# Performance work log

Measured on AMD Instinct MI355X. Metric: run time of the kernel, lower is better.

## Reference

```python
import jax, jax.numpy as jnp
import numpy as np

EPS = 1e-6


def _safe_norm(x, axis, keepdims=True):
    # sqrt with zero-safe gradient (double-where trick)
    sq = (x * x).sum(axis=axis, keepdims=keepdims)
    safe = jnp.where(sq > 0, sq, 1.0)
    return jnp.where(sq > 0, jnp.sqrt(safe), 0.0)


def _complex_coord_norm(lig, pro, lig_mask, pro_mask, set_weights):
    # 'length' norm over the joint complex: scale each set so the mean vector
    # length over all real (lig + pro) nodes is ~1, with a learnable per-set weight.
    lig_len = _safe_norm(lig, axis=-1, keepdims=False) * lig_mask   # [B,S,Nl]
    pro_len = _safe_norm(pro, axis=-1, keepdims=False) * pro_mask   # [B,S,Np]
    total_len = lig_len.sum(-1) + pro_len.sum(-1)                   # [B,S]
    n_atoms = lig_mask.sum(-1) + pro_mask.sum(-1)                   # [B,S]
    mean_len = (total_len / n_atoms)[..., None, None]               # [B,S,1,1]
    w = set_weights[None, :, None, None]
    lig = lig * w / (mean_len + EPS) * lig_mask[..., None]
    pro = pro * w / (mean_len + EPS) * pro_mask[..., None]
    return lig, pro


def setup_inputs() -> dict:
    key = jax.random.key(0)
    ks = jax.random.split(key, 8)
    B, S, P, Nl, Np = 8, 64, 64, 128, 256
    scale = 1.0 / np.sqrt(S)
    return {
        "lig_coord_sets": jax.random.normal(ks[0], (B, S, Nl, 3), jnp.float32),
        "messages": jax.random.normal(ks[1], (B, Nl, Nl + Np, P), jnp.float32),
        "adj_matrix": jax.random.randint(ks[2], (B, Nl, Nl + Np), 0, 2, jnp.int32),
        "lig_node_mask": jnp.ones((B, S, Nl), jnp.float32),
        "pro_coord_sets": jax.random.normal(ks[3], (B, S, Np, 3), jnp.float32),
        "pro_node_mask": jnp.ones((B, S, Np), jnp.float32),
        "lig_proj_w": jax.random.normal(ks[4], (P, S), jnp.float32) * scale,
        "pro_proj_w": jax.random.normal(ks[5], (P, S), jnp.float32) * scale,
        "attn_proj_w": jax.random.normal(ks[6], (S, P), jnp.float32) * scale,
        "set_weights": jnp.ones((S,), jnp.float32),
    }


def reference(lig_coord_sets, messages, adj_matrix, lig_node_mask,
              pro_coord_sets, pro_node_mask,
              lig_proj_w, pro_proj_w, attn_proj_w, set_weights):
    B, S, Nl, _ = lig_coord_sets.shape
    lig, pro = _complex_coord_norm(lig_coord_sets, pro_coord_sets,
                                   lig_node_mask, pro_node_mask, set_weights)
    # Linear over the sets dim: [B,S,N,3] -> [B,3,N,P]
    lig_p = jnp.einsum('bsnc,ps->bcnp', lig, lig_proj_w)
    pro_p = jnp.einsum('bsnc,ps->bcnp', pro, pro_proj_w)
    proj = jnp.concatenate([lig_p, pro_p], axis=2)        # [B,3,N,P]
    # pairwise vector diffs, ligand queries only (matches post-hoc slice in torch)
    vec = proj[:, :, :Nl, None, :] - proj[:, :, None, :, :]   # [B,3,Nl,N,P]
    lengths = _safe_norm(vec, axis=1)                          # [B,1,Nl,N,P]
    norm_dists = vec / (lengths + EPS)
    attn_mask = jnp.where(adj_matrix > 0, 0.0, -jnp.inf)       # [B,Nl,N]
    attn = jax.nn.softmax(messages + attn_mask[..., None], axis=2)  # [B,Nl,N,P]
    upd = jnp.einsum('bcinp,binp->bcip', norm_dists, attn)     # [B,3,Nl,P]
    weights = jnp.sqrt((attn * attn).sum(axis=2))              # [B,Nl,P]
    upd = upd * weights[:, None]
    # attn_proj (P -> S) + transpose(1,-1): [B,3,Nl,P] -> [B,S,Nl,3]
    return jnp.einsum('bcip,sp->bsic', upd, attn_proj_w)
```

## Files before the change

kernel.cpp:

```cpp
#include <hip/hip_runtime.h>
#include <hip/hip_bf16.h>
#include <math.h>

#define B   8
#define S   64
#define NL  128
#define NPRO 256
#define NN  384
#define P   64
#define NGRP 8
#define EPSF 1e-6f

__global__ __launch_bounds__(64) void meanlen_kernel(
    const float* __restrict__ lig, const float* __restrict__ ligmask,
    const float* __restrict__ pro, const float* __restrict__ promask,
    float* __restrict__ meanlen)
{
    int blk = blockIdx.x;
    int t = threadIdx.x;
    float suml = 0.f, cnt = 0.f;

    const float* lbase = lig + (size_t)blk * NL * 3;
    const float* lm    = ligmask + (size_t)blk * NL;
    for (int n = t; n < NL; n += 64) {
        float x = lbase[n*3+0], y = lbase[n*3+1], z = lbase[n*3+2];
        float mk = lm[n];
        suml += sqrtf(x*x + y*y + z*z) * mk;
        cnt  += mk;
    }
    const float* pbase = pro + (size_t)blk * NPRO * 3;
    const float* pm    = promask + (size_t)blk * NPRO;
    for (int n = t; n < NPRO; n += 64) {
        float x = pbase[n*3+0], y = pbase[n*3+1], z = pbase[n*3+2];
        float mk = pm[n];
        suml += sqrtf(x*x + y*y + z*z) * mk;
        cnt  += mk;
    }
    for (int off = 32; off > 0; off >>= 1) {
        suml += __shfl_down(suml, off);
        cnt  += __shfl_down(cnt,  off);
    }
    if (t == 0) meanlen[blk] = suml / cnt;
}

__global__ __launch_bounds__(64) void proj_kernel(
    const float* __restrict__ lig, const float* __restrict__ pro,
    const float* __restrict__ ligmask, const float* __restrict__ promask,
    const float* __restrict__ ligw, const float* __restrict__ prow,
    const float* __restrict__ sw, const float* __restrict__ meanlen,
    float* __restrict__ projx, float* __restrict__ projy, float* __restrict__ projz)
{
    int blk = blockIdx.x;
    int b = blk / (NN / NGRP);
    int g = blk - b * (NN / NGRP);
    int nbase = g * NGRP;
    int t = threadIdx.x;
    bool isl = (nbase < NL);

    __shared__ float wl[64][65];
    const float* w = isl ? ligw : prow;
    for (int row = 0; row < 64; ++row) wl[row][t] = w[row * 64 + t];

    __shared__ float cs[NGRP][3][64];
    {
        int s = t;
        float gfac = sw[s] / (meanlen[b * S + s] + EPSF);
        for (int nn = 0; nn < NGRP; ++nn) {
            int n = nbase + nn;
            float mk, X, Y, Z;
            if (isl) {
                size_t base = ((size_t)b * S + s) * NL + n;
                mk = ligmask[base];
                X = lig[base*3+0]; Y = lig[base*3+1]; Z = lig[base*3+2];
            } else {
                size_t base = ((size_t)b * S + s) * NPRO + (n - NL);
                mk = promask[base];
                X = pro[base*3+0]; Y = pro[base*3+1]; Z = pro[base*3+2];
            }
            float gg = gfac * mk;
            cs[nn][0][s] = X * gg;
            cs[nn][1][s] = Y * gg;
            cs[nn][2][s] = Z * gg;
        }
    }
    __syncthreads();

    for (int nn = 0; nn < NGRP; ++nn) {
        float a0 = 0.f, a1 = 0.f, a2 = 0.f;
        #pragma unroll 8
        for (int s = 0; s < 64; ++s) {
            float wv = wl[t][s];
            a0 += cs[nn][0][s] * wv;
            a1 += cs[nn][1][s] * wv;
            a2 += cs[nn][2][s] * wv;
        }
        size_t base = ((size_t)b * NN + nbase + nn) * P;
        projx[base + t] = a0;
        projy[base + t] = a1;
        projz[base + t] = a2;
    }
}

#define PROC(C) { \
    float d0 = xix.C - xx.C, d1 = xiy.C - yy.C, d2 = xiz.C - zz.C; \
    float sq = fmaf(d0, d0, fmaf(d1, d1, d2 * d2)); \
    float inv; asm("v_rsq_f32 %0, %1" : "=v"(inv) : "v"(sq)); \
    inv = sq > 0.f ? inv : 0.f; \
    float xe = fmaf(mm.C, 1.44269504f, am); \
    float e; asm("v_exp_f32 %0, %1" : "=v"(e) : "v"(xe)); \
    S1.C += e; S2.C = fmaf(e, e, S2.C); \
    float ei = e * inv; \
    A0.C = fmaf(ei, d0, A0.C); \
    A1.C = fmaf(ei, d1, A1.C); \
    A2.C = fmaf(ei, d2, A2.C); }

#define RED(V) { V.x += __shfl_xor(V.x, off); V.y += __shfl_xor(V.y, off); \
                 V.z += __shfl_xor(V.z, off); V.w += __shfl_xor(V.w, off); }

__global__ __launch_bounds__(512) void attn_kernel(
    const float* __restrict__ messages,
    const int*   __restrict__ adj,
    const float* __restrict__ projx,
    const float* __restrict__ projy,
    const float* __restrict__ projz,
    const float* __restrict__ attn_w,
    float* __restrict__ out)
{
    int blk = blockIdx.x;
    int b = blk >> 7;
    int i = blk & (NL - 1);
    int t = threadIdx.x;
    int lane = t & 63;
    int wave = t >> 6;
    int pg = lane & 15;
    int wsl = lane >> 4;
    int slice = wave * 4 + wsl;

    __shared__ float amask[NN];
    __shared__ float ls1[8][64], ls2[8][64];
    __shared__ float la0[8][64], la1[8][64], la2[8][64];
    __shared__ float upd[3][64];

    const int* adj_base = adj + (size_t)blk * NN;
    for (int n = t; n < NN; n += 512)
        amask[n] = adj_base[n] > 0 ? 0.f : -INFINITY;

    const float4* m4  = (const float4*)messages + (size_t)blk * NN * 16;
    const float4* px4 = (const float4*)projx + (size_t)b * NN * 16;
    const float4* py4 = (const float4*)projy + (size_t)b * NN * 16;
    const float4* pz4 = (const float4*)projz + (size_t)b * NN * 16;

    float4 xix = px4[(size_t)i * 16 + pg];
    float4 xiy = py4[(size_t)i * 16 + pg];
    float4 xiz = pz4[(size_t)i * 16 + pg];

    __syncthreads();

    float4 S1 = {0,0,0,0}, S2 = {0,0,0,0};
    float4 A0 = {0,0,0,0}, A1 = {0,0,0,0}, A2 = {0,0,0,0};

    int nb = slice * 12;
    size_t idx0 = (size_t)nb * 16 + pg;
    float4 mc = m4[idx0], xc = px4[idx0], yc = py4[idx0], zc = pz4[idx0];

    #pragma unroll
    for (int k = 0; k < 12; ++k) {
        int n = nb + k;
        float4 mm = mc, xx = xc, yy = yc, zz = zc;
        if (k < 11) {
            size_t idx = (size_t)(n + 1) * 16 + pg;
            mc = m4[idx]; xc = px4[idx]; yc = py4[idx]; zc = pz4[idx];
        }
        float am = amask[n];
        PROC(x) PROC(y) PROC(z) PROC(w)
    }

    #pragma unroll
    for (int off = 16; off <= 32; off <<= 1) {
        RED(S1) RED(S2) RED(A0) RED(A1) RED(A2)
    }

    if (wsl == 0) {
        int pbase = pg * 4;
        ls1[wave][pbase+0] = S1.x; ls1[wave][pbase+1] = S1.y; ls1[wave][pbase+2] = S1.z; ls1[wave][pbase+3] = S1.w;
        ls2[wave][pbase+0] = S2.x; ls2[wave][pbase+1] = S2.y; ls2[wave][pbase+2] = S2.z; ls2[wave][pbase+3] = S2.w;
        la0[wave][pbase+0] = A0.x; la0[wave][pbase+1] = A0.y; la0[wave][pbase+2] = A0.z; la0[wave][pbase+3] = A0.w;
        la1[wave][pbase+0] = A1.x; la1[wave][pbase+1] = A1.y; la1[wave][pbase+2] = A1.z; la1[wave][pbase+3] = A1.w;
        la2[wave][pbase+0] = A2.x; la2[wave][pbase+1] = A2.y; la2[wave][pbase+2] = A2.z; la2[wave][pbase+3] = A2.w;
    }
    __syncthreads();

    if (t < 64) {
        float s1 = 0.f, s2 = 0.f, a0 = 0.f, a1 = 0.f, a2 = 0.f;
        #pragma unroll
        for (int w = 0; w < 8; ++w) {
            s1 += ls1[w][t]; s2 += ls2[w][t];
            a0 += la0[w][t]; a1 += la1[w][t]; a2 += la2[w][t];
        }
        float wgt = sqrtf(s2) / (s1 * s1);
        upd[0][t] = a0 * wgt;
        upd[1][t] = a1 * wgt;
        upd[2][t] = a2 * wgt;
    }
    __syncthreads();

    if (t < 192) {
        int s = t & 63, c = t >> 6;
        const float4* aw4 = (const float4*)attn_w + (size_t)s * 16;
        float o = 0.f;
        #pragma unroll
        for (int q = 0; q < 16; ++q) {
            float4 w4 = aw4[q];
            o = fmaf(upd[c][q*4+0], w4.x, o);
            o = fmaf(upd[c][q*4+1], w4.y, o);
            o = fmaf(upd[c][q*4+2], w4.z, o);
            o = fmaf(upd[c][q*4+3], w4.w, o);
        }
        out[(((size_t)b * S + s) * NL + i) * 3 + c] = o;
    }
}

extern "C" void kernel_launch(void* const* d_in, const int* in_sizes, int n_in,
                              void* d_out, int out_size, void* d_ws, size_t ws_size,
                              hipStream_t stream)
{
    const float* lig      = (const float*)d_in[0];
    const float* messages = (const float*)d_in[1];
    const int*   adj      = (const int*)  d_in[2];
    const float* ligmask  = (const float*)d_in[3];
    const float* pro      = (const float*)d_in[4];
    const float* promask  = (const float*)d_in[5];
    const float* ligw     = (const float*)d_in[6];
    const float* prow     = (const float*)d_in[7];
    const float* attnw    = (const float*)d_in[8];
    const float* sw       = (const float*)d_in[9];
    float* out = (float*)d_out;

    const size_t plane = (size_t)B * NN * P;
    float* meanlen = (float*)d_ws;
    float* projx   = (float*)((char*)d_ws + 2048);
    float* projy   = projx + plane;
    float* projz   = projy + plane;

    meanlen_kernel<<<B * S, 64, 0, stream>>>(lig, ligmask, pro, promask, meanlen);
    proj_kernel<<<B * (NN / NGRP), 64, 0, stream>>>(lig, pro, ligmask, promask,
                                                    ligw, prow, sw, meanlen,
                                                    projx, projy, projz);
    attn_kernel<<<B * NL, 512, 0, stream>>>(messages, adj, projx, projy, projz,
                                            attnw, out);
}
```

Baseline: 53.80 us.

## Process two query rows per attention block to reuse projected neighbor loads

The attention kernel now handles two ligand query rows per block, sharing the loads of projected neighbor coordinates between them and halving the grid. Prefetching is deepened to two iterations, and the zero-length guard is replaced by clamping rsq with fminf. This reduces redundant L2 reads of the proj planes and per-block overhead, at the cost of doubled accumulator registers and possibly lower occupancy.

```diff
diff --git a/kernel.cpp b/kernel.cpp
--- a/kernel.cpp
+++ b/kernel.cpp
@@ -101,18 +101,25 @@
     }
 }
 
-#define PROC(C) { \
-    float d0 = xix.C - xx.C, d1 = xiy.C - yy.C, d2 = xiz.C - zz.C; \
+#define PROC2(C) { \
+    float d0 = xi0x.C - xx.C, d1 = xi0y.C - yy.C, d2 = xi0z.C - zz.C; \
     float sq = fmaf(d0, d0, fmaf(d1, d1, d2 * d2)); \
     float inv; asm("v_rsq_f32 %0, %1" : "=v"(inv) : "v"(sq)); \
-    inv = sq > 0.f ? inv : 0.f; \
-    float xe = fmaf(mm.C, 1.44269504f, am); \
+    inv = fminf(inv, 1e30f); \
+    float xe = fmaf(mm0.C, 1.44269504f, am0); \
     float e; asm("v_exp_f32 %0, %1" : "=v"(e) : "v"(xe)); \
-    S1.C += e; S2.C = fmaf(e, e, S2.C); \
+    S1a.C += e; S2a.C = fmaf(e, e, S2a.C); \
     float ei = e * inv; \
-    A0.C = fmaf(ei, d0, A0.C); \
-    A1.C = fmaf(ei, d1, A1.C); \
-    A2.C = fmaf(ei, d2, A2.C); }
+    A0a.C = fmaf(ei, d0, A0a.C); A1a.C = fmaf(ei, d1, A1a.C); A2a.C = fmaf(ei, d2, A2a.C); \
+    d0 = xi1x.C - xx.C; d1 = xi1y.C - yy.C; d2 = xi1z.C - zz.C; \
+    sq = fmaf(d0, d0, fmaf(d1, d1, d2 * d2)); \
+    asm("v_rsq_f32 %0, %1" : "=v"(inv) : "v"(sq)); \
+    inv = fminf(inv, 1e30f); \
+    xe = fmaf(mm1.C, 1.44269504f, am1); \
+    asm("v_exp_f32 %0, %1" : "=v"(e) : "v"(xe)); \
+    S1b.C += e; S2b.C = fmaf(e, e, S2b.C); \
+    ei = e * inv; \
+    A0b.C = fmaf(ei, d0, A0b.C); A1b.C = fmaf(ei, d1, A1b.C); A2b.C = fmaf(ei, d2, A2b.C); }
 
 #define RED(V) { V.x += __shfl_xor(V.x, off); V.y += __shfl_xor(V.y, off); \
                  V.z += __shfl_xor(V.z, off); V.w += __shfl_xor(V.w, off); }
@@ -127,8 +134,10 @@
     float* __restrict__ out)
 {
     int blk = blockIdx.x;
-    int b = blk >> 7;
-    int i = blk & (NL - 1);
+    int b = blk >> 6;
+    int ip = blk & 63;
+    int i0 = ip * 2;
+    int i1 = i0 + 1;
     int t = threadIdx.x;
     int lane = t & 63;
     int wave = t >> 6;
@@ -136,85 +145,104 @@
     int wsl = lane >> 4;
     int slice = wave * 4 + wsl;
 
-    __shared__ float amask[NN];
-    __shared__ float ls1[8][64], ls2[8][64];
-    __shared__ float la0[8][64], la1[8][64], la2[8][64];
-    __shared__ float upd[3][64];
-
-    const int* adj_base = adj + (size_t)blk * NN;
-    for (int n = t; n < NN; n += 512)
-        amask[n] = adj_base[n] > 0 ? 0.f : -INFINITY;
-
-    const float4* m4  = (const float4*)messages + (size_t)blk * NN * 16;
+    __shared__ float amask[2][NN];
+    __shared__ __align__(16) float red[2][5][8][64];
+    __shared__ float upd[2][3][64];
+
+    const int* adj0 = adj + ((size_t)b * NL + i0) * NN;
+    const int* adj1 = adj + ((size_t)b * NL + i1) * NN;
+    for (int n = t; n < NN; n += 512) {
+        amask[0][n] = adj0[n] > 0 ? 0.f : -INFINITY;
+        amask[1][n] = adj1[n] > 0 ? 0.f : -INFINITY;
+    }
+
+    const float4* m04 = (const float4*)messages + ((size_t)b * NL + i0) * NN * 16;
+    const float4* m14 = (const float4*)messages + ((size_t)b * NL + i1) * NN * 16;
     const float4* px4 = (const float4*)projx + (size_t)b * NN * 16;
     const float4* py4 = (const float4*)projy + (size_t)b * NN * 16;
     const float4* pz4 = (const float4*)projz + (size_t)b * NN * 16;
 
-    float4 xix = px4[(size_t)i * 16 + pg];
-    float4 xiy = py4[(size_t)i * 16 + pg];
-    float4 xiz = pz4[(size_t)i * 16 + pg];
-
-    __syncthreads();
-
-    float4 S1 = {0,0,0,0}, S2 = {0,0,0,0};
-    float4 A0 = {0,0,0,0}, A1 = {0,0,0,0}, A2 = {0,0,0,0};
+    float4 xi0x = px4[(size_t)i0 * 16 + pg];
+    float4 xi0y = py4[(size_t)i0 * 16 + pg];
+    float4 xi0z = pz4[(size_t)i0 * 16 + pg];
+    float4 xi1x = px4[(size_t)i1 * 16 + pg];
+    float4 xi1y = py4[(size_t)i1 * 16 + pg];
+    float4 xi1z = pz4[(size_t)i1 * 16 + pg];
+
+    __syncthreads();
+
+    float4 S1a = {0,0,0,0}, S2a = {0,0,0,0}, A0a = {0,0,0,0}, A1a = {0,0,0,0}, A2a = {0,0,0,0};
+    float4 S1b = {0,0,0,0}, S2b = {0,0,0,0}, A0b = {0,0,0,0}, A1b = {0,0,0,0}, A2b = {0,0,0,0};
 
     int nb = slice * 12;
-    size_t idx0 = (size_t)nb * 16 + pg;
-    float4 mc = m4[idx0], xc = px4[idx0], yc = py4[idx0], zc = pz4[idx0];
+    size_t base = (size_t)nb * 16 + pg;
+
+    float4 bm0[2], bm1[2], bx[2], by[2], bz[2];
+    bm0[0] = m04[base];      bm1[0] = m14[base];
+    bx[0]  = px4[base];      by[0]  = py4[base];      bz[0] = pz4[base];
+    bm0[1] = m04[base + 16]; bm1[1] = m14[base + 16];
+    bx[1]  = px4[base + 16]; by[1]  = py4[base + 16]; bz[1] = pz4[base + 16];
 
     #pragma unroll
     for (int k = 0; k < 12; ++k) {
+        float4 mm0 = bm0[k & 1], mm1 = bm1[k & 1];
+        float4 xx = bx[k & 1], yy = by[k & 1], zz = bz[k & 1];
+        if (k < 10) {
+            size_t idx = base + (size_t)(k + 2) * 16;
+            bm0[k & 1] = m04[idx]; bm1[k & 1] = m14[idx];
+            bx[k & 1]  = px4[idx]; by[k & 1]  = py4[idx]; bz[k & 1] = pz4[idx];
+        }
         int n = nb + k;
-        float4 mm = mc, xx = xc, yy = yc, zz = zc;
-        if (k < 11) {
-            size_t idx = (size_t)(n + 1) * 16 + pg;
-            mc = m4[idx]; xc = px4[idx]; yc = py4[idx]; zc = pz4[idx];
-        }
-        float am = amask[n];
-        PROC(x) PROC(y) PROC(z) PROC(w)
+        float am0 = amask[0][n], am1 = amask[1][n];
+        PROC2(x) PROC2(y) PROC2(z) PROC2(w)
     }
 
     #pragma unroll
     for (int off = 16; off <= 32; off <<= 1) {
-        RED(S1) RED(S2) RED(A0) RED(A1) RED(A2)
+        RED(S1a) RED(S2a) RED(A0a) RED(A1a) RED(A2a)
+        RED(S1b) RED(S2b) RED(A0b) RED(A1b) RED(A2b)
     }
 
     if (wsl == 0) {
-        int pbase = pg * 4;
-        ls1[wave][pbase+0] = S1.x; ls1[wave][pbase+1] = S1.y; ls1[wave][pbase+2] = S1.z; ls1[wave][pbase+3] = S1.w;
-        ls2[wave][pbase+0] = S2.x; ls2[wave][pbase+1] = S2.y; ls2[wave][pbase+2] = S2.z; ls2[wave][pbase+3] = S2.w;
-        la0[wave][pbase+0] = A0.x; la0[wave][pbase+1] = A0.y; la0[wave][pbase+2] = A0.z; la0[wave][pbase+3] = A0.w;
-        la1[wave][pbase+0] = A1.x; la1[wave][pbase+1] = A1.y; la1[wave][pbase+2] = A1.z; la1[wave][pbase+3] = A1.w;
-        la2[wave][pbase+0] = A2.x; la2[wave][pbase+1] = A2.y; la2[wave][pbase+2] = A2.z; la2[wave][pbase+3] = A2.w;
-    }
-    __syncthreads();
-
-    if (t < 64) {
+        int pb = pg * 4;
+        *(float4*)&red[0][0][wave][pb] = S1a; *(float4*)&red[0][1][wave][pb] = S2a;
+        *(float4*)&red[0][2][wave][pb] = A0a; *(float4*)&red[0][3][wave][pb] = A1a;
+        *(float4*)&red[0][4][wave][pb] = A2a;
+        *(float4*)&red[1][0][wave][pb] = S1b; *(float4*)&red[1][1][wave][pb] = S2b;
+        *(float4*)&red[1][2][wave][pb] = A0b; *(float4*)&red[1][3][wave][pb] = A1b;
+        *(float4*)&red[1][4][wave][pb] = A2b;
+    }
+    __syncthreads();
+
+    if (t < 128) {
+        int il = t >> 6, p = t & 63;
         float s1 = 0.f, s2 = 0.f, a0 = 0.f, a1 = 0.f, a2 = 0.f;
         #pragma unroll
         for (int w = 0; w < 8; ++w) {
-            s1 += ls1[w][t]; s2 += ls2[w][t];
-            a0 += la0[w][t]; a1 += la1[w][t]; a2 += la2[w][t];
+            s1 += red[il][0][w][p]; s2 += red[il][1][w][p];
+            a0 += red[il][2][w][p]; a1 += red[il][3][w][p]; a2 += red[il][4][w][p];
         }
         float wgt = sqrtf(s2) / (s1 * s1);
-        upd[0][t] = a0 * wgt;
-        upd[1][t] = a1 * wgt;
-        upd[2][t] = a2 * wgt;
-    }
-    __syncthreads();
-
-    if (t < 192) {
-        int s = t & 63, c = t >> 6;
+        upd[il][0][p] = a0 * wgt;
+        upd[il][1][p] = a1 * wgt;
+        upd[il][2][p] = a2 * wgt;
+    }
+    __syncthreads();
+
+    if (t < 384) {
+        int il = t >= 192;
+        int r = t - il * 192;
+        int s = r & 63, c = r >> 6;
+        int i = i0 + il;
         const float4* aw4 = (const float4*)attn_w + (size_t)s * 16;
         float o = 0.f;
         #pragma unroll
         for (int q = 0; q < 16; ++q) {
             float4 w4 = aw4[q];
-            o = fmaf(upd[c][q*4+0], w4.x, o);
-            o = fmaf(upd[c][q*4+1], w4.y, o);
-            o = fmaf(upd[c][q*4+2], w4.z, o);
-            o = fmaf(upd[c][q*4+3], w4.w, o);
+            o = fmaf(upd[il][c][q*4+0], w4.x, o);
+            o = fmaf(upd[il][c][q*4+1], w4.y, o);
+            o = fmaf(upd[il][c][q*4+2], w4.z, o);
+            o = fmaf(upd[il][c][q*4+3], w4.w, o);
         }
         out[(((size_t)b * S + s) * NL + i) * 3 + c] = o;
     }
@@ -246,6 +274,6 @@
     proj_kernel<<<B * (NN / NGRP), 64, 0, stream>>>(lig, pro, ligmask, promask,
                                                     ligw, prow, sw, meanlen,
                                                     projx, projy, projz);
-    attn_kernel<<<B * NL, 512, 0, stream>>>(messages, adj, projx, projy, projz,
-                                            attnw, out);
-}
+    attn_kernel<<<B * NL / 2, 512, 0, stream>>>(messages, adj, projx, projy, projz,
+                                                attnw, out);
+}
```

New measurement: 52.88 us. Within noise of the previous version (-1.7%).

## Stream messages through double-buffered LDS tiles via global_load_lds in attn kernel

Applied to the files above, without the earlier changes.

The attention kernel now uses 256 threads per block and streams the messages tensor in 32-node tiles into double-buffered shared memory with direct global-to-LDS loads, prefetching the next tile while the current one is processed. Each 16-thread group handles two nodes per tile, and the cross-wave reduction buffers are packed into one float4-written array. The zero-length guard becomes a clamp of the rsq result. The intent is to hide latency on the dominant messages read. It adds a block-wide barrier per tile and halves the threads per block.

```diff
diff --git a/kernel.cpp b/kernel.cpp
--- a/kernel.cpp
+++ b/kernel.cpp
@@ -101,23 +101,24 @@
     }
 }
 
-#define PROC(C) { \
+#define NTILE 32
+#define TILES (NN / NTILE)
+
+#define PROC(mm, am, xx, yy, zz, C) { \
     float d0 = xix.C - xx.C, d1 = xiy.C - yy.C, d2 = xiz.C - zz.C; \
     float sq = fmaf(d0, d0, fmaf(d1, d1, d2 * d2)); \
     float inv; asm("v_rsq_f32 %0, %1" : "=v"(inv) : "v"(sq)); \
-    inv = sq > 0.f ? inv : 0.f; \
+    inv = fminf(inv, 1e30f); \
     float xe = fmaf(mm.C, 1.44269504f, am); \
     float e; asm("v_exp_f32 %0, %1" : "=v"(e) : "v"(xe)); \
     S1.C += e; S2.C = fmaf(e, e, S2.C); \
     float ei = e * inv; \
-    A0.C = fmaf(ei, d0, A0.C); \
-    A1.C = fmaf(ei, d1, A1.C); \
-    A2.C = fmaf(ei, d2, A2.C); }
+    A0.C = fmaf(ei, d0, A0.C); A1.C = fmaf(ei, d1, A1.C); A2.C = fmaf(ei, d2, A2.C); }
 
 #define RED(V) { V.x += __shfl_xor(V.x, off); V.y += __shfl_xor(V.y, off); \
                  V.z += __shfl_xor(V.z, off); V.w += __shfl_xor(V.w, off); }
 
-__global__ __launch_bounds__(512) void attn_kernel(
+__global__ __launch_bounds__(256) void attn_kernel(
     const float* __restrict__ messages,
     const int*   __restrict__ adj,
     const float* __restrict__ projx,
@@ -132,20 +133,20 @@
     int t = threadIdx.x;
     int lane = t & 63;
     int wave = t >> 6;
-    int pg = lane & 15;
+    int pg  = t & 15;
+    int sub = t >> 4;
     int wsl = lane >> 4;
-    int slice = wave * 4 + wsl;
 
     __shared__ float amask[NN];
-    __shared__ float ls1[8][64], ls2[8][64];
-    __shared__ float la0[8][64], la1[8][64], la2[8][64];
+    __shared__ __align__(16) float msgT[2][NTILE * P];
+    __shared__ __align__(16) float red[4][5][64];
     __shared__ float upd[3][64];
 
-    const int* adj_base = adj + (size_t)blk * NN;
-    for (int n = t; n < NN; n += 512)
-        amask[n] = adj_base[n] > 0 ? 0.f : -INFINITY;
-
-    const float4* m4  = (const float4*)messages + (size_t)blk * NN * 16;
+    const int* adjb = adj + (size_t)blk * NN;
+    for (int n = t; n < NN; n += 256)
+        amask[n] = adjb[n] > 0 ? 0.f : -INFINITY;
+
+    const float* msgb = messages + (size_t)blk * NN * P;
     const float4* px4 = (const float4*)projx + (size_t)b * NN * 16;
     const float4* py4 = (const float4*)projy + (size_t)b * NN * 16;
     const float4* pz4 = (const float4*)projz + (size_t)b * NN * 16;
@@ -154,25 +155,43 @@
     float4 xiy = py4[(size_t)i * 16 + pg];
     float4 xiz = pz4[(size_t)i * 16 + pg];
 
+    #define STAGE(buf, tile) { \
+        const char* gs = (const char*)(msgb + (size_t)(tile) * (NTILE * P)); \
+        char* ls = (char*)&msgT[buf][0] + wave * 2048; \
+        unsigned lo = wave * 2048 + lane * 16; \
+        __builtin_amdgcn_global_load_lds((const unsigned int*)(gs + lo), \
+                                         (unsigned int*)ls, 16, 0, 0); \
+        __builtin_amdgcn_global_load_lds((const unsigned int*)(gs + lo + 1024), \
+                                         (unsigned int*)(ls + 1024), 16, 0, 0); \
+    }
+
+    STAGE(0, 0)
     __syncthreads();
 
     float4 S1 = {0,0,0,0}, S2 = {0,0,0,0};
     float4 A0 = {0,0,0,0}, A1 = {0,0,0,0}, A2 = {0,0,0,0};
 
-    int nb = slice * 12;
-    size_t idx0 = (size_t)nb * 16 + pg;
-    float4 mc = m4[idx0], xc = px4[idx0], yc = py4[idx0], zc = pz4[idx0];
-
+    int cur = 0;
     #pragma unroll
-    for (int k = 0; k < 12; ++k) {
-        int n = nb + k;
-        float4 mm = mc, xx = xc, yy = yc, zz = zc;
-        if (k < 11) {
-            size_t idx = (size_t)(n + 1) * 16 + pg;
-            mc = m4[idx]; xc = px4[idx]; yc = py4[idx]; zc = pz4[idx];
-        }
-        float am = amask[n];
-        PROC(x) PROC(y) PROC(z) PROC(w)
+    for (int tile = 0; tile < TILES; ++tile) {
+        if (tile < TILES - 1) STAGE(cur ^ 1, tile + 1)
+
+        int n0 = tile * NTILE + sub * 2;
+        float4 mA = *(const float4*)&msgT[cur][(sub * 2    ) * P + pg * 4];
+        float4 mB = *(const float4*)&msgT[cur][(sub * 2 + 1) * P + pg * 4];
+        float amA = amask[n0], amB = amask[n0 + 1];
+
+        size_t gA = (size_t)n0 * 16 + pg;
+        float4 xA = px4[gA],      yA = py4[gA],      zA = pz4[gA];
+        float4 xB = px4[gA + 16], yB = py4[gA + 16], zB = pz4[gA + 16];
+
+        PROC(mA, amA, xA, yA, zA, x) PROC(mA, amA, xA, yA, zA, y)
+        PROC(mA, amA, xA, yA, zA, z) PROC(mA, amA, xA, yA, zA, w)
+        PROC(mB, amB, xB, yB, zB, x) PROC(mB, amB, xB, yB, zB, y)
+        PROC(mB, amB, xB, yB, zB, z) PROC(mB, amB, xB, yB, zB, w)
+
+        __syncthreads();
+        cur ^= 1;
     }
 
     #pragma unroll
@@ -181,21 +200,19 @@
     }
 
     if (wsl == 0) {
-        int pbase = pg * 4;
-        ls1[wave][pbase+0] = S1.x; ls1[wave][pbase+1] = S1.y; ls1[wave][pbase+2] = S1.z; ls1[wave][pbase+3] = S1.w;
-        ls2[wave][pbase+0] = S2.x; ls2[wave][pbase+1] = S2.y; ls2[wave][pbase+2] = S2.z; ls2[wave][pbase+3] = S2.w;
-        la0[wave][pbase+0] = A0.x; la0[wave][pbase+1] = A0.y; la0[wave][pbase+2] = A0.z; la0[wave][pbase+3] = A0.w;
-        la1[wave][pbase+0] = A1.x; la1[wave][pbase+1] = A1.y; la1[wave][pbase+2] = A1.z; la1[wave][pbase+3] = A1.w;
-        la2[wave][pbase+0] = A2.x; la2[wave][pbase+1] = A2.y; la2[wave][pbase+2] = A2.z; la2[wave][pbase+3] = A2.w;
+        int pb = pg * 4;
+        *(float4*)&red[wave][0][pb] = S1; *(float4*)&red[wave][1][pb] = S2;
+        *(float4*)&red[wave][2][pb] = A0; *(float4*)&red[wave][3][pb] = A1;
+        *(float4*)&red[wave][4][pb] = A2;
     }
     __syncthreads();
 
     if (t < 64) {
         float s1 = 0.f, s2 = 0.f, a0 = 0.f, a1 = 0.f, a2 = 0.f;
         #pragma unroll
-        for (int w = 0; w < 8; ++w) {
-            s1 += ls1[w][t]; s2 += ls2[w][t];
-            a0 += la0[w][t]; a1 += la1[w][t]; a2 += la2[w][t];
+        for (int w = 0; w < 4; ++w) {
+            s1 += red[w][0][t]; s2 += red[w][1][t];
+            a0 += red[w][2][t]; a1 += red[w][3][t]; a2 += red[w][4][t];
         }
         float wgt = sqrtf(s2) / (s1 * s1);
         upd[0][t] = a0 * wgt;
@@ -246,6 +263,6 @@
     proj_kernel<<<B * (NN / NGRP), 64, 0, stream>>>(lig, pro, ligmask, promask,
                                                     ligw, prow, sw, meanlen,
                                                     projx, projy, projz);
-    attn_kernel<<<B * NL, 512, 0, stream>>>(messages, adj, projx, projy, projz,
+    attn_kernel<<<B * NL, 256, 0, stream>>>(messages, adj, projx, projy, projz,
                                             attnw, out);
 }
```

After: 55.73 us. +3.6%, slower.

## Split attention into N-chunked partial kernel with register-cached neighbor projections plus combine

Applied to the files above, without the earlier changes.

The single attention kernel is replaced by a partial kernel and a combine kernel. The partial kernel tiles over 16 query rows and 48 neighbors per block, keeping the neighbor projections in registers and reusing them across the 16 queries. It writes per-chunk partial sums to workspace, and a second kernel reduces them and applies the output projection. This cuts repeated reads of the projection data, at the cost of an extra launch, a partial-buffer round trip through memory, a syncthreads per query row, and only 512 blocks in the partial kernel. The masked-zero case now uses fminf on rsq instead of a select.

```diff
diff --git a/kernel.cpp b/kernel.cpp
--- a/kernel.cpp
+++ b/kernel.cpp
@@ -101,28 +101,87 @@
     }
 }
 
-#define PROC(C) { \
-    float d0 = xix.C - xx.C, d1 = xiy.C - yy.C, d2 = xiz.C - zz.C; \
-    float sq = fmaf(d0, d0, fmaf(d1, d1, d2 * d2)); \
-    float inv; asm("v_rsq_f32 %0, %1" : "=v"(inv) : "v"(sq)); \
-    inv = sq > 0.f ? inv : 0.f; \
-    float xe = fmaf(mm.C, 1.44269504f, am); \
-    float e; asm("v_exp_f32 %0, %1" : "=v"(e) : "v"(xe)); \
-    S1.C += e; S2.C = fmaf(e, e, S2.C); \
-    float ei = e * inv; \
-    A0.C = fmaf(ei, d0, A0.C); \
-    A1.C = fmaf(ei, d1, A1.C); \
-    A2.C = fmaf(ei, d2, A2.C); }
-
-#define RED(V) { V.x += __shfl_xor(V.x, off); V.y += __shfl_xor(V.y, off); \
-                 V.z += __shfl_xor(V.z, off); V.w += __shfl_xor(V.w, off); }
-
-__global__ __launch_bounds__(512) void attn_kernel(
+__global__ __launch_bounds__(256) void partial_kernel(
     const float* __restrict__ messages,
     const int*   __restrict__ adj,
     const float* __restrict__ projx,
     const float* __restrict__ projy,
     const float* __restrict__ projz,
+    float* __restrict__ partial)
+{
+    int blk = blockIdx.x;
+    int b  = blk >> 6;
+    int nh = (blk >> 3) & 7;
+    int ic = blk & 7;
+    int t = threadIdx.x;
+    int wave = t >> 6;
+    int p = t & 63;
+    int n0 = nh * 48 + wave * 12;
+
+    __shared__ float amk[16][48];
+    __shared__ float wavepart[2][4][5][64];
+
+    for (int idx = t; idx < 16 * 48; idx += 256) {
+        int il = idx / 48, q = idx - il * 48;
+        amk[il][q] = adj[((size_t)b * NL + ic * 16 + il) * NN + nh * 48 + q] > 0
+                     ? 0.f : -INFINITY;
+    }
+
+    float xnx[12], xny[12], xnz[12];
+    size_t pbase = ((size_t)b * NN + n0) * 64 + p;
+    #pragma unroll
+    for (int k = 0; k < 12; ++k) {
+        xnx[k] = projx[pbase + (size_t)k * 64];
+        xny[k] = projy[pbase + (size_t)k * 64];
+        xnz[k] = projz[pbase + (size_t)k * 64];
+    }
+    __syncthreads();
+
+    #pragma unroll 1
+    for (int il = 0; il < 16; ++il) {
+        size_t row = (size_t)b * NL + ic * 16 + il;
+        size_t xidx = ((size_t)b * NN + ic * 16 + il) * 64 + p;
+        float xix = projx[xidx], xiy = projy[xidx], xiz = projz[xidx];
+
+        const float* mb = messages + (row * NN + n0) * 64 + p;
+        float m[12];
+        #pragma unroll
+        for (int k = 0; k < 12; ++k) m[k] = mb[(size_t)k * 64];
+
+        float s1 = 0.f, s2 = 0.f, a0 = 0.f, a1 = 0.f, a2 = 0.f;
+        #pragma unroll
+        for (int k = 0; k < 12; ++k) {
+            float am = amk[il][wave * 12 + k];
+            float d0 = xix - xnx[k], d1 = xiy - xny[k], d2 = xiz - xnz[k];
+            float sq = fmaf(d0, d0, fmaf(d1, d1, d2 * d2));
+            float inv; asm("v_rsq_f32 %0, %1" : "=v"(inv) : "v"(sq));
+            inv = fminf(inv, 1e30f);
+            float xe = fmaf(m[k], 1.44269504f, am);
+            float e; asm("v_exp_f32 %0, %1" : "=v"(e) : "v"(xe));
+            float ei = e * inv;
+            s1 += e; s2 = fmaf(e, e, s2);
+            a0 = fmaf(ei, d0, a0); a1 = fmaf(ei, d1, a1); a2 = fmaf(ei, d2, a2);
+        }
+
+        int buf = il & 1;
+        wavepart[buf][wave][0][p] = s1;
+        wavepart[buf][wave][1][p] = s2;
+        wavepart[buf][wave][2][p] = a0;
+        wavepart[buf][wave][3][p] = a1;
+        wavepart[buf][wave][4][p] = a2;
+        __syncthreads();
+
+        for (int idx = t; idx < 320; idx += 256) {
+            int acc = idx >> 6, pp = idx & 63;
+            float v = wavepart[buf][0][acc][pp] + wavepart[buf][1][acc][pp]
+                    + wavepart[buf][2][acc][pp] + wavepart[buf][3][acc][pp];
+            partial[((row * 8 + nh) * 5 + acc) * 64 + pp] = v;
+        }
+    }
+}
+
+__global__ __launch_bounds__(192) void combine_kernel(
+    const float* __restrict__ partial,
     const float* __restrict__ attn_w,
     float* __restrict__ out)
 {
@@ -130,72 +189,19 @@
     int b = blk >> 7;
     int i = blk & (NL - 1);
     int t = threadIdx.x;
-    int lane = t & 63;
-    int wave = t >> 6;
-    int pg = lane & 15;
-    int wsl = lane >> 4;
-    int slice = wave * 4 + wsl;
-
-    __shared__ float amask[NN];
-    __shared__ float ls1[8][64], ls2[8][64];
-    __shared__ float la0[8][64], la1[8][64], la2[8][64];
+
     __shared__ float upd[3][64];
-
-    const int* adj_base = adj + (size_t)blk * NN;
-    for (int n = t; n < NN; n += 512)
-        amask[n] = adj_base[n] > 0 ? 0.f : -INFINITY;
-
-    const float4* m4  = (const float4*)messages + (size_t)blk * NN * 16;
-    const float4* px4 = (const float4*)projx + (size_t)b * NN * 16;
-    const float4* py4 = (const float4*)projy + (size_t)b * NN * 16;
-    const float4* pz4 = (const float4*)projz + (size_t)b * NN * 16;
-
-    float4 xix = px4[(size_t)i * 16 + pg];
-    float4 xiy = py4[(size_t)i * 16 + pg];
-    float4 xiz = pz4[(size_t)i * 16 + pg];
-
-    __syncthreads();
-
-    float4 S1 = {0,0,0,0}, S2 = {0,0,0,0};
-    float4 A0 = {0,0,0,0}, A1 = {0,0,0,0}, A2 = {0,0,0,0};
-
-    int nb = slice * 12;
-    size_t idx0 = (size_t)nb * 16 + pg;
-    float4 mc = m4[idx0], xc = px4[idx0], yc = py4[idx0], zc = pz4[idx0];
-
-    #pragma unroll
-    for (int k = 0; k < 12; ++k) {
-        int n = nb + k;
-        float4 mm = mc, xx = xc, yy = yc, zz = zc;
-        if (k < 11) {
-            size_t idx = (size_t)(n + 1) * 16 + pg;
-            mc = m4[idx]; xc = px4[idx]; yc = py4[idx]; zc = pz4[idx];
-        }
-        float am = amask[n];
-        PROC(x) PROC(y) PROC(z) PROC(w)
-    }
-
-    #pragma unroll
-    for (int off = 16; off <= 32; off <<= 1) {
-        RED(S1) RED(S2) RED(A0) RED(A1) RED(A2)
-    }
-
-    if (wsl == 0) {
-        int pbase = pg * 4;
-        ls1[wave][pbase+0] = S1.x; ls1[wave][pbase+1] = S1.y; ls1[wave][pbase+2] = S1.z; ls1[wave][pbase+3] = S1.w;
-        ls2[wave][pbase+0] = S2.x; ls2[wave][pbase+1] = S2.y; ls2[wave][pbase+2] = S2.z; ls2[wave][pbase+3] = S2.w;
-        la0[wave][pbase+0] = A0.x; la0[wave][pbase+1] = A0.y; la0[wave][pbase+2] = A0.z; la0[wave][pbase+3] = A0.w;
-        la1[wave][pbase+0] = A1.x; la1[wave][pbase+1] = A1.y; la1[wave][pbase+2] = A1.z; la1[wave][pbase+3] = A1.w;
-        la2[wave][pbase+0] = A2.x; la2[wave][pbase+1] = A2.y; la2[wave][pbase+2] = A2.z; la2[wave][pbase+3] = A2.w;
-    }
-    __syncthreads();
 
     if (t < 64) {
         float s1 = 0.f, s2 = 0.f, a0 = 0.f, a1 = 0.f, a2 = 0.f;
         #pragma unroll
-        for (int w = 0; w < 8; ++w) {
-            s1 += ls1[w][t]; s2 += ls2[w][t];
-            a0 += la0[w][t]; a1 += la1[w][t]; a2 += la2[w][t];
+        for (int nh = 0; nh < 8; ++nh) {
+            size_t base = (((size_t)blk * 8 + nh) * 5) * 64 + t;
+            s1 += partial[base];
+            s2 += partial[base + 64];
+            a0 += partial[base + 128];
+            a1 += partial[base + 192];
+            a2 += partial[base + 256];
         }
         float wgt = sqrtf(s2) / (s1 * s1);
         upd[0][t] = a0 * wgt;
@@ -204,20 +210,18 @@
     }
     __syncthreads();
 
-    if (t < 192) {
-        int s = t & 63, c = t >> 6;
-        const float4* aw4 = (const float4*)attn_w + (size_t)s * 16;
-        float o = 0.f;
-        #pragma unroll
-        for (int q = 0; q < 16; ++q) {
-            float4 w4 = aw4[q];
-            o = fmaf(upd[c][q*4+0], w4.x, o);
-            o = fmaf(upd[c][q*4+1], w4.y, o);
-            o = fmaf(upd[c][q*4+2], w4.z, o);
-            o = fmaf(upd[c][q*4+3], w4.w, o);
-        }
-        out[(((size_t)b * S + s) * NL + i) * 3 + c] = o;
-    }
+    int s = t & 63, c = t >> 6;
+    const float4* aw4 = (const float4*)attn_w + (size_t)s * 16;
+    float o = 0.f;
+    #pragma unroll
+    for (int q = 0; q < 16; ++q) {
+        float4 w4 = aw4[q];
+        o = fmaf(upd[c][q*4+0], w4.x, o);
+        o = fmaf(upd[c][q*4+1], w4.y, o);
+        o = fmaf(upd[c][q*4+2], w4.z, o);
+        o = fmaf(upd[c][q*4+3], w4.w, o);
+    }
+    out[(((size_t)b * S + s) * NL + i) * 3 + c] = o;
 }
 
 extern "C" void kernel_launch(void* const* d_in, const int* in_sizes, int n_in,
@@ -241,11 +245,13 @@
     float* projx   = (float*)((char*)d_ws + 2048);
     float* projy   = projx + plane;
     float* projz   = projy + plane;
+    float* partial = (float*)((char*)d_ws + (4u << 20));
 
     meanlen_kernel<<<B * S, 64, 0, stream>>>(lig, ligmask, pro, promask, meanlen);
     proj_kernel<<<B * (NN / NGRP), 64, 0, stream>>>(lig, pro, ligmask, promask,
                                                     ligw, prow, sw, meanlen,
                                                     projx, projy, projz);
-    attn_kernel<<<B * NL, 512, 0, stream>>>(messages, adj, projx, projy, projz,
-                                            attnw, out);
-}
+    partial_kernel<<<B * 8 * 8, 256, 0, stream>>>(messages, adj,
+                                                  projx, projy, projz, partial);
+    combine_kernel<<<B * NL, 192, 0, stream>>>(partial, attnw, out);
+}
```

After: 59.86 us. 1.11x slower.
